# Optimization experiments

Hardware: AMD Instinct MI355X
Metric: run time of the kernel (lower is better)

## Reference

```python
import jax, jax.numpy as jnp
import numpy as np

DIM = 128
BATCH = 8192
# Static index sets (constants, mirror diag_ind / tril_ind / diag_ind_tril)
TRIL_R, TRIL_C = np.tril_indices(DIM)          # row/col of lower-tri entries, row-major
DIAG_IN_TRIL = np.nonzero(TRIL_R == TRIL_C)[0]  # positions of diagonal entries in flat tril vector
DIAG = np.arange(DIM)
N_TRIL = TRIL_R.size  # dim*(dim+1)/2 = 8256


def setup_inputs() -> dict:
    key = jax.random.key(0)
    x = jax.random.normal(key, (BATCH, N_TRIL), dtype=jnp.float32)
    return {"x": x}


def reference(x):
    # Scatter-fill batched lower-triangular matrix L: [..., DIM, DIM]
    batch_shape = x.shape[:-1]
    L = jnp.zeros(batch_shape + (DIM, DIM), dtype=x.dtype)
    L = L.at[..., TRIL_R, TRIL_C].set(x)
    # Overwrite diagonal with log1p(exp(x_diag) + 1e-12) (softplus-like, as in source)
    diag = jnp.log1p(jnp.exp(x[..., DIAG_IN_TRIL]) + 1e-12)
    L = L.at[..., DIAG, DIAG].set(diag)
    # Diffusion matrix L @ L^T
    return jnp.einsum('...ik,...jk->...ij', L, L)
```

## Files before the change

### kernel.cpp

```cpp
#include <hip/hip_runtime.h>
#include <math.h>


#define DIM        128
#define NTRIL      8256
#define LDS_STRIDE 136
#define ROW_BYTES  272

typedef __bf16 bf16x8 __attribute__((ext_vector_type(8)));
typedef float  f32x16 __attribute__((ext_vector_type(16)));

struct RcTab { unsigned short off[NTRIL]; };
static constexpr RcTab make_tab() {
    RcTab t{};
    int idx = 0;
    for (int r = 0; r < DIM; ++r)
        for (int c = 0; c <= r; ++c)
            t.off[idx++] = (unsigned short)((r * LDS_STRIDE + c) * 2);
    return t;
}
__device__ const RcTab TBL = make_tab();

__global__ __launch_bounds__(256) void tril2diff_kernel(
    const float* __restrict__ x, float* __restrict__ out)
{
    __shared__ alignas(16) __bf16 Lsh[DIM * LDS_STRIDE];

    const int b   = blockIdx.x;
    const int tid = threadIdx.x;

    uint4* lz4 = (uint4*)Lsh;
    #pragma unroll
    for (int i = 0; i < 8; ++i)
        lz4[tid + i * 256] = uint4{0u, 0u, 0u, 0u};
    if (tid < 128)
        lz4[2048 + tid] = uint4{0u, 0u, 0u, 0u};
    __syncthreads();

    const float* xb = x + (size_t)b * NTRIL;
    char* lbw = (char*)Lsh;
    #pragma unroll
    for (int i = 0; i < 8; ++i) {
        const int t4 = (tid + i * 256) * 4;
        const float4  v = *(const float4*)(xb + t4);
        const ushort4 o = *(const ushort4*)(TBL.off + t4);
        *(__bf16*)(lbw + o.x) = (__bf16)v.x;
        *(__bf16*)(lbw + o.y) = (__bf16)v.y;
        *(__bf16*)(lbw + o.z) = (__bf16)v.z;
        *(__bf16*)(lbw + o.w) = (__bf16)v.w;
    }
    if (tid < 16) {
        const int t4 = (2048 + tid) * 4;
        const float4  v = *(const float4*)(xb + t4);
        const ushort4 o = *(const ushort4*)(TBL.off + t4);
        *(__bf16*)(lbw + o.x) = (__bf16)v.x;
        *(__bf16*)(lbw + o.y) = (__bf16)v.y;
        *(__bf16*)(lbw + o.z) = (__bf16)v.z;
        *(__bf16*)(lbw + o.w) = (__bf16)v.w;
    }
    __syncthreads();

    if (tid < DIM) {
        const int r = tid;
        const int t = (r * (r + 1)) / 2 + r;
        float v = xb[t];
        v = log1pf(expf(v) + 1e-12f);
        Lsh[r * LDS_STRIDE + r] = (__bf16)v;
    }
    __syncthreads();

    const int lane = tid & 63;
    const int wv   = tid >> 6;
    const int i0   = (wv >> 1) * 64;
    const int j0   = (wv & 1) * 64;
    const int cl   = lane & 31;
    const int hh   = lane >> 5;

    f32x16 acc00 = {0}, acc01 = {0}, acc10 = {0}, acc11 = {0};
    const char* lb = (const char*)Lsh;

#define MFMA_STEP(ks)                                                          \
    {                                                                          \
        const int koff = (ks) * 32 + hh * 16;                                  \
        bf16x8 a0 = *(const bf16x8*)(lb + (i0      + cl) * ROW_BYTES + koff);  \
        bf16x8 a1 = *(const bf16x8*)(lb + (i0 + 32 + cl) * ROW_BYTES + koff);  \
        bf16x8 b0 = *(const bf16x8*)(lb + (j0      + cl) * ROW_BYTES + koff);  \
        bf16x8 b1 = *(const bf16x8*)(lb + (j0 + 32 + cl) * ROW_BYTES + koff);  \
        acc00 = __builtin_amdgcn_mfma_f32_32x32x16_bf16(a0, b0, acc00, 0, 0, 0); \
        acc01 = __builtin_amdgcn_mfma_f32_32x32x16_bf16(a0, b1, acc01, 0, 0, 0); \
        acc10 = __builtin_amdgcn_mfma_f32_32x32x16_bf16(a1, b0, acc10, 0, 0, 0); \
        acc11 = __builtin_amdgcn_mfma_f32_32x32x16_bf16(a1, b1, acc11, 0, 0, 0); \
    }

    #pragma unroll
    for (int ks = 0; ks < 4; ++ks)
        MFMA_STEP(ks);
    if (wv == 3) {
        #pragma unroll
        for (int ks = 4; ks < 8; ++ks)
            MFMA_STEP(ks);
    }
#undef MFMA_STEP

    float* ob = out + (size_t)b * (DIM * DIM);
    #pragma unroll
    for (int reg = 0; reg < 16; ++reg) {
        const int row = (reg & 3) + 8 * (reg >> 2) + 4 * hh;
        ob[(i0      + row) * DIM + j0      + cl] = acc00[reg];
        ob[(i0      + row) * DIM + j0 + 32 + cl] = acc01[reg];
        ob[(i0 + 32 + row) * DIM + j0      + cl] = acc10[reg];
        ob[(i0 + 32 + row) * DIM + j0 + 32 + cl] = acc11[reg];
    }
}

extern "C" void kernel_launch(void* const* d_in, const int* in_sizes, int n_in,
                              void* d_out, int out_size, void* d_ws, size_t ws_size,
                              hipStream_t stream) {
    const float* x = (const float*)d_in[0];
    float* out = (float*)d_out;
    const int batch = in_sizes[0] / NTRIL;
    tril2diff_kernel<<<batch, 256, 0, stream>>>(x, out);
}
```

Before: 687.6 us.

## Swizzle LDS layout with XOR and issue global loads before zero-fill

Replaces the padded LDS row stride with an unpadded 256-byte row whose 16-byte chunks are XOR-swizzled by row index. This aims to avoid bank conflicts on the MFMA operand reads while shrinking LDS use. All global loads of x, the offset table and the diagonal value now happen up front, before the LDS zero-fill and barrier, so their latency overlaps that work. The diagonal softplus is computed before the barrier. The cost is more live registers, which could lower occupancy.

After: 680.7 us. No clear change (-1.0%).

```diff
diff --git a/kernel.cpp b/kernel.cpp
--- a/kernel.cpp
+++ b/kernel.cpp
@@ -4,8 +4,7 @@
 
 #define DIM        128
 #define NTRIL      8256
-#define LDS_STRIDE 136
-#define ROW_BYTES  272
+#define ROW_BYTES  256
 
 typedef __bf16 bf16x8 __attribute__((ext_vector_type(8)));
 typedef float  f32x16 __attribute__((ext_vector_type(16)));
@@ -16,57 +15,69 @@
     int idx = 0;
     for (int r = 0; r < DIM; ++r)
         for (int c = 0; c <= r; ++c)
-            t.off[idx++] = (unsigned short)((r * LDS_STRIDE + c) * 2);
+            t.off[idx++] = (unsigned short)((r * ROW_BYTES + c * 2) ^ ((r & 7) << 4));
     return t;
 }
 __device__ const RcTab TBL = make_tab();
 
+__device__ __forceinline__ int rowbase(int r) {
+    return (r << 8) ^ ((r & 7) << 4);
+}
+
 __global__ __launch_bounds__(256) void tril2diff_kernel(
     const float* __restrict__ x, float* __restrict__ out)
 {
-    __shared__ alignas(16) __bf16 Lsh[DIM * LDS_STRIDE];
+    __shared__ alignas(16) __bf16 Lsh[DIM * ROW_BYTES / 2];
 
     const int b   = blockIdx.x;
     const int tid = threadIdx.x;
+    const float* xb = x + (size_t)b * NTRIL;
+
+    float4  v[8];
+    ushort4 o[8];
+    #pragma unroll
+    for (int i = 0; i < 8; ++i) {
+        const int t4 = (tid + i * 256) * 4;
+        v[i] = *(const float4*)(xb + t4);
+        o[i] = *(const ushort4*)(TBL.off + t4);
+    }
+    float4 vt; ushort4 ot;
+    if (tid < 16) {
+        const int t4 = (2048 + tid) * 4;
+        vt = *(const float4*)(xb + t4);
+        ot = *(const ushort4*)(TBL.off + t4);
+    }
+    float dvx;
+    if (tid < DIM)
+        dvx = xb[(tid * (tid + 1)) / 2 + tid];
 
     uint4* lz4 = (uint4*)Lsh;
     #pragma unroll
     for (int i = 0; i < 8; ++i)
         lz4[tid + i * 256] = uint4{0u, 0u, 0u, 0u};
-    if (tid < 128)
-        lz4[2048 + tid] = uint4{0u, 0u, 0u, 0u};
     __syncthreads();
 
-    const float* xb = x + (size_t)b * NTRIL;
     char* lbw = (char*)Lsh;
     #pragma unroll
     for (int i = 0; i < 8; ++i) {
-        const int t4 = (tid + i * 256) * 4;
-        const float4  v = *(const float4*)(xb + t4);
-        const ushort4 o = *(const ushort4*)(TBL.off + t4);
-        *(__bf16*)(lbw + o.x) = (__bf16)v.x;
-        *(__bf16*)(lbw + o.y) = (__bf16)v.y;
-        *(__bf16*)(lbw + o.z) = (__bf16)v.z;
-        *(__bf16*)(lbw + o.w) = (__bf16)v.w;
+        *(__bf16*)(lbw + o[i].x) = (__bf16)v[i].x;
+        *(__bf16*)(lbw + o[i].y) = (__bf16)v[i].y;
+        *(__bf16*)(lbw + o[i].z) = (__bf16)v[i].z;
+        *(__bf16*)(lbw + o[i].w) = (__bf16)v[i].w;
     }
     if (tid < 16) {
-        const int t4 = (2048 + tid) * 4;
-        const float4  v = *(const float4*)(xb + t4);
-        const ushort4 o = *(const ushort4*)(TBL.off + t4);
-        *(__bf16*)(lbw + o.x) = (__bf16)v.x;
-        *(__bf16*)(lbw + o.y) = (__bf16)v.y;
-        *(__bf16*)(lbw + o.z) = (__bf16)v.z;
-        *(__bf16*)(lbw + o.w) = (__bf16)v.w;
+        *(__bf16*)(lbw + ot.x) = (__bf16)vt.x;
+        *(__bf16*)(lbw + ot.y) = (__bf16)vt.y;
+        *(__bf16*)(lbw + ot.z) = (__bf16)vt.z;
+        *(__bf16*)(lbw + ot.w) = (__bf16)vt.w;
     }
+    float dv;
+    if (tid < DIM)
+        dv = log1pf(expf(dvx) + 1e-12f);
     __syncthreads();
 
-    if (tid < DIM) {
-        const int r = tid;
-        const int t = (r * (r + 1)) / 2 + r;
-        float v = xb[t];
-        v = log1pf(expf(v) + 1e-12f);
-        Lsh[r * LDS_STRIDE + r] = (__bf16)v;
-    }
+    if (tid < DIM)
+        *(__bf16*)(lbw + ((tid * ROW_BYTES + tid * 2) ^ ((tid & 7) << 4))) = (__bf16)dv;
     __syncthreads();
 
     const int lane = tid & 63;
@@ -75,17 +86,23 @@
     const int j0   = (wv & 1) * 64;
     const int cl   = lane & 31;
     const int hh   = lane >> 5;
+    const int kb   = hh * 16;
+
+    const int ba0 = rowbase(i0      + cl);
+    const int ba1 = rowbase(i0 + 32 + cl);
+    const int bb0 = rowbase(j0      + cl);
+    const int bb1 = rowbase(j0 + 32 + cl);
 
     f32x16 acc00 = {0}, acc01 = {0}, acc10 = {0}, acc11 = {0};
     const char* lb = (const char*)Lsh;
 
 #define MFMA_STEP(ks)                                                          \
     {                                                                          \
-        const int koff = (ks) * 32 + hh * 16;                                  \
-        bf16x8 a0 = *(const bf16x8*)(lb + (i0      + cl) * ROW_BYTES + koff);  \
-        bf16x8 a1 = *(const bf16x8*)(lb + (i0 + 32 + cl) * ROW_BYTES + koff);  \
-        bf16x8 b0 = *(const bf16x8*)(lb + (j0      + cl) * ROW_BYTES + koff);  \
-        bf16x8 b1 = *(const bf16x8*)(lb + (j0 + 32 + cl) * ROW_BYTES + koff);  \
+        const int koff = (ks) * 32 + kb;                                       \
+        bf16x8 a0 = *(const bf16x8*)(lb + (ba0 ^ koff));                       \
+        bf16x8 a1 = *(const bf16x8*)(lb + (ba1 ^ koff));                       \
+        bf16x8 b0 = *(const bf16x8*)(lb + (bb0 ^ koff));                       \
+        bf16x8 b1 = *(const bf16x8*)(lb + (bb1 ^ koff));                       \
         acc00 = __builtin_amdgcn_mfma_f32_32x32x16_bf16(a0, b0, acc00, 0, 0, 0); \
         acc01 = __builtin_amdgcn_mfma_f32_32x32x16_bf16(a0, b1, acc01, 0, 0, 0); \
         acc10 = __builtin_amdgcn_mfma_f32_32x32x16_bf16(a1, b0, acc10, 0, 0, 0); \
```
